# Kernel tuning notes

Measured on AMD Instinct MI355X. Metric: run time of the kernel, lower is better.

Reference implementation:

```python
import jax, jax.numpy as jnp
import numpy as np

B, N, K, D, H = 4, 8192, 16, 128, 4
DK = D // H  # key_dim = num_hiddens // num_heads
NEG_INF = -1e9


def setup_inputs() -> dict:
    key = jax.random.key(0)
    ks = jax.random.split(key, 16)
    s = 1.0 / np.sqrt(D)
    return {
        "vertex_feat": jax.random.normal(ks[0], (B, N, D), dtype=jnp.float32),
        "neighbors_idx": jax.random.randint(ks[1], (B, N, K), 0, N, dtype=jnp.int32),
        "valid_lens": jax.random.randint(ks[2], (B, N), 0, K, dtype=jnp.int32),
        # MultiHeadAttention projections (keras EinsumDense with bias)
        "Wq": (jax.random.normal(ks[3], (D, H, DK)) * s).astype(jnp.float32),
        "bq": jnp.zeros((H, DK), jnp.float32),
        "Wk": (jax.random.normal(ks[4], (D, H, DK)) * s).astype(jnp.float32),
        "bk": jnp.zeros((H, DK), jnp.float32),
        "Wv": (jax.random.normal(ks[5], (D, H, DK)) * s).astype(jnp.float32),
        "bv": jnp.zeros((H, DK), jnp.float32),
        "Wo": (jax.random.normal(ks[6], (H, DK, D)) * s).astype(jnp.float32),
        "bo": jnp.zeros((D,), jnp.float32),
        # MLP: Dense(D, relu) -> Dense(D)
        "W1": (jax.random.normal(ks[7], (D, D)) * s).astype(jnp.float32),
        "b1": jnp.zeros((D,), jnp.float32),
        "W2": (jax.random.normal(ks[8], (D, D)) * s).astype(jnp.float32),
        "b2": jnp.zeros((D,), jnp.float32),
    }


def reference(vertex_feat, neighbors_idx, valid_lens,
              Wq, bq, Wk, bk, Wv, bv, Wo, bo, W1, b1, W2, b2):
    # query: [B, N, 1, D]; gathered neighbors (batch_dims=1): [B, N, K, D]
    q = vertex_feat[:, :, None, :]
    neigh = jax.vmap(lambda vf, idx: vf[idx])(vertex_feat, neighbors_idx)
    value = jnp.concatenate([q, neigh], axis=2)  # [B, N, K+1, D]

    # per-head projections
    qh = jnp.einsum('bnqd,dhk->bnqhk', q, Wq) + bq      # [B,N,1,H,DK]
    kh = jnp.einsum('bnsd,dhk->bnshk', value, Wk) + bk  # [B,N,K+1,H,DK]
    vh = jnp.einsum('bnsd,dhk->bnshk', value, Wv) + bv

    # attention over the neighbor axis (attention_axes=(2,))
    scores = jnp.einsum('bnqhk,bnshk->bnhqs', qh, kh) / np.sqrt(DK)  # [B,N,H,1,K+1]
    # mask: positions < valid_lens + 1 (self + valid neighbors)
    pos = jnp.arange(K + 1)[None, None, :]                # [1,1,K+1]
    mask = pos < (valid_lens + 1)[:, :, None]             # [B,N,K+1] bool
    scores = scores + jnp.where(mask, 0.0, NEG_INF)[:, :, None, None, :]
    attn = jax.nn.softmax(scores, axis=-1)                # [B,N,H,1,K+1]

    ctx = jnp.einsum('bnhqs,bnshk->bnqhk', attn, vh)      # [B,N,1,H,DK]
    out = jnp.einsum('bnqhk,hkd->bnqd', ctx, Wo) + bo     # [B,N,1,D]
    out = out[:, :, 0, :]                                  # squeeze -> [B,N,D]

    # MLP (dropout inactive at inference)
    h = jax.nn.relu(out @ W1 + b1)
    new_vertex_feat = h @ W2 + b2
    return new_vertex_feat
```

## Files before the change

### kernel.cpp

```cpp
#include <hip/hip_runtime.h>
#include <math.h>

#define BB 4
#define NN 8192
#define KNB 16
#define DD 128
#define SS 17
#define M_TOT (BB*NN)
#define WPAD 136

typedef __attribute__((ext_vector_type(8))) short          bf8;
typedef __attribute__((ext_vector_type(4))) float          f4;
typedef __attribute__((ext_vector_type(4))) unsigned short u16x4;

static __device__ __forceinline__ unsigned short f2bf(float f) {
    unsigned u = __builtin_bit_cast(unsigned, f);
    u += 0x7fffu + ((u >> 16) & 1u);
    return (unsigned short)(u >> 16);
}
static __device__ __forceinline__ float bf2f_s(short h) {
    return __builtin_bit_cast(float, (unsigned)(unsigned short)h << 16);
}

__global__ __launch_bounds__(256) void cvt_wT(
    const float* __restrict__ Wq, const float* __restrict__ Wk,
    const float* __restrict__ Wv, const float* __restrict__ Wo,
    const float* __restrict__ W1, const float* __restrict__ W2,
    unsigned short* __restrict__ out)
{
    int m = blockIdx.x >> 4;
    const float* src = (m == 0) ? Wq : (m == 1) ? Wk : (m == 2) ? Wv
                     : (m == 3) ? Wo : (m == 4) ? W1 : W2;
    unsigned short* dst = out + m * 16384;
    int o = (blockIdx.x & 15) * 1024 + threadIdx.x * 4;
    int n = o >> 7, k = o & 127;
    u16x4 r;
    #pragma unroll
    for (int i = 0; i < 4; ++i) r[i] = f2bf(src[(size_t)(k + i) * 128 + n]);
    *(u16x4*)(dst + o) = r;
}

__global__ __launch_bounds__(256) void qkv_kernel(
    const float* __restrict__ X, const unsigned short* __restrict__ WtT,
    const float* __restrict__ bq, const float* __restrict__ bk,
    const float* __restrict__ bv,
    unsigned short* __restrict__ qh, unsigned short* __restrict__ kv)
{
    __shared__ unsigned short Xs[64 * WPAD];
    __shared__ unsigned short Wb[128 * WPAD];

    const int tid  = threadIdx.x;
    const int row0 = blockIdx.x * 64;

    {
        const float4* Xg = (const float4*)(X + (size_t)row0 * DD);
        #pragma unroll
        for (int i = 0; i < 8; ++i) {
            int idx = tid + i * 256;
            int r = idx >> 5, c4 = idx & 31;
            float4 v = Xg[idx];
            u16x4 u;
            u[0] = f2bf(v.x); u[1] = f2bf(v.y); u[2] = f2bf(v.z); u[3] = f2bf(v.w);
            *(u16x4*)(Xs + r * WPAD + c4 * 4) = u;
        }
    }
    #pragma unroll
    for (int i = 0; i < 8; ++i) {
        int c = tid + i * 256;
        int n = c >> 4, k8 = c & 15;
        *(bf8*)(Wb + n * WPAD + k8 * 8) = ((const bf8*)WtT)[c];
    }

    const int lane = tid & 63, wv = tid >> 6;
    const int ln = lane & 15, quad = lane >> 4;
    __syncthreads();

    bf8 afr[4];
    #pragma unroll
    for (int s = 0; s < 4; ++s)
        afr[s] = *(const bf8*)(Xs + (wv * 16 + ln) * WPAD + s * 32 + quad * 8);

    const float* biases[3] = { bq, bk, bv };
    unsigned short* outs[3] = { qh, kv, kv + 128 };
    const int strides[3] = { 128, 256, 256 };

    #pragma unroll 1
    for (int g = 0; g < 3; ++g) {
        if (g > 0) {
            __syncthreads();
            const bf8* Wn = (const bf8*)(WtT + g * 16384);
            #pragma unroll
            for (int i = 0; i < 8; ++i) {
                int c = tid + i * 256;
                int n = c >> 4, k8 = c & 15;
                *(bf8*)(Wb + n * WPAD + k8 * 8) = Wn[c];
            }
            __syncthreads();
        }

        f4 acc[8] = {};
        #pragma unroll
        for (int t = 0; t < 8; ++t) {
            bf8 bfr[4];
            #pragma unroll
            for (int s = 0; s < 4; ++s)
                bfr[s] = *(const bf8*)(Wb + (t * 16 + ln) * WPAD + s * 32 + quad * 8);
            #pragma unroll
            for (int s = 0; s < 4; ++s)
                acc[t] = __builtin_amdgcn_mfma_f32_16x16x32_bf16(afr[s], bfr[s], acc[t], 0, 0, 0);
        }

        const float* bias = biases[g];
        unsigned short* Y = outs[g];
        const int st = strides[g];
        #pragma unroll
        for (int t = 0; t < 8; ++t) {
            int col = t * 16 + ln;
            float bc = bias[col];
            #pragma unroll
            for (int r = 0; r < 4; ++r) {
                int row = row0 + wv * 16 + quad * 4 + r;
                Y[(size_t)row * st + col] = f2bf(acc[t][r] + bc);
            }
        }
    }
}

__global__ __launch_bounds__(256) void attn_kernel(
    const unsigned short* __restrict__ Qh, const unsigned short* __restrict__ KV,
    const int* __restrict__ nbr, const int* __restrict__ vlen,
    unsigned short* __restrict__ Ctx)
{
    const int tid  = threadIdx.x;
    const int vloc = tid >> 5;
    const int sp   = (tid >> 4) & 1;
    const int ln16 = tid & 15;
    const int blk  = blockIdx.x;
    const int b    = (blk & 7) >> 1;
    const int j    = ((blk >> 3) << 1) | (blk & 1);
    const int v    = b * NN + j * 8 + vloc;
    const int len  = vlen[v];

    bf8 q8 = *(const bf8*)(Qh + (size_t)v * DD + ln16 * 8);
    float qf[8];
    #pragma unroll
    for (int i = 0; i < 8; ++i) qf[i] = bf2f_s(q8[i]);

    int rows[9];
    {
        const int4* np = (const int4*)(nbr + (size_t)v * KNB);
        if (sp == 0) {
            rows[0] = v;
            int4 a = np[0], c = np[1];
            rows[1] = b * NN + a.x; rows[2] = b * NN + a.y;
            rows[3] = b * NN + a.z; rows[4] = b * NN + a.w;
            rows[5] = b * NN + c.x; rows[6] = b * NN + c.y;
            rows[7] = b * NN + c.z; rows[8] = b * NN + c.w;
        } else {
            int4 a = np[2], c = np[3];
            rows[0] = b * NN + a.x; rows[1] = b * NN + a.y;
            rows[2] = b * NN + a.z; rows[3] = b * NN + a.w;
            rows[4] = b * NN + c.x; rows[5] = b * NN + c.y;
            rows[6] = b * NN + c.z; rows[7] = b * NN + c.w;
            rows[8] = v;
        }
    }
    const int s0 = sp * 9;

    bf8 k8[9];
    #pragma unroll
    for (int i = 0; i < 9; ++i)
        k8[i] = *(const bf8*)(KV + (size_t)rows[i] * 256 + ln16 * 8);

    float sc[9];
    #pragma unroll
    for (int i = 0; i < 9; ++i) {
        float p = 0.f;
        #pragma unroll
        for (int d = 0; d < 8; ++d) p = fmaf(qf[d], bf2f_s(k8[i][d]), p);
        p += __shfl_xor(p, 1, 4);
        p += __shfl_xor(p, 2, 4);
        sc[i] = (s0 + i <= len) ? p * 0.17677669529663687f : -1.0e9f;
    }

    bf8 v8[9];
    #pragma unroll
    for (int i = 0; i < 9; ++i)
        v8[i] = *(const bf8*)(KV + (size_t)rows[i] * 256 + 128 + ln16 * 8);

    float m = sc[0];
    #pragma unroll
    for (int i = 1; i < 9; ++i) m = fmaxf(m, sc[i]);
    m = fmaxf(m, __shfl_xor(m, 16));
    float sum = 0.f;
    #pragma unroll
    for (int i = 0; i < 9; ++i) {
        float e = __expf(sc[i] - m);
        sc[i] = e;
        sum += e;
    }
    sum += __shfl_xor(sum, 16);
    const float inv = 1.f / sum;

    float acc[8] = {};
    #pragma unroll
    for (int i = 0; i < 9; ++i) {
        float w = sc[i] * inv;
        #pragma unroll
        for (int d = 0; d < 8; ++d) acc[d] = fmaf(w, bf2f_s(v8[i][d]), acc[d]);
    }
    #pragma unroll
    for (int d = 0; d < 8; ++d) acc[d] += __shfl_xor(acc[d], 16);

    if (sp == 0) {
        bf8 r;
        #pragma unroll
        for (int d = 0; d < 8; ++d) r[d] = (short)f2bf(acc[d]);
        *(bf8*)(Ctx + (size_t)v * DD + ln16 * 8) = r;
    }
}

__global__ __launch_bounds__(256) void ffn_kernel(
    const unsigned short* __restrict__ Ctxg, const unsigned short* __restrict__ WtT3,
    const float* __restrict__ bo, const float* __restrict__ b1,
    const float* __restrict__ b2, float* __restrict__ Out)
{
    __shared__ unsigned short Ct[64 * WPAD];
    __shared__ unsigned short Wb[128 * WPAD];

    const int tid  = threadIdx.x;
    const int row0 = blockIdx.x * 64;

    {
        const bf8* Cg = (const bf8*)(Ctxg + (size_t)row0 * DD);
        #pragma unroll
        for (int i = 0; i < 4; ++i) {
            int idx = tid + i * 256;
            int r = idx >> 4, c8 = idx & 15;
            *(bf8*)(Ct + r * WPAD + c8 * 8) = Cg[idx];
        }
    }
    #pragma unroll
    for (int i = 0; i < 8; ++i) {
        int c = tid + i * 256;
        int n = c >> 4, k8 = c & 15;
        *(bf8*)(Wb + n * WPAD + k8 * 8) = ((const bf8*)WtT3)[c];
    }

    const int lane = tid & 63, wv = tid >> 6;
    const int ln = lane & 15, quad = lane >> 4;
    const float* biases[3] = { bo, b1, b2 };
    __syncthreads();

    #pragma unroll 1
    for (int g = 0; g < 3; ++g) {
        bf8 afr[4];
        #pragma unroll
        for (int s = 0; s < 4; ++s)
            afr[s] = *(const bf8*)(Ct + (wv * 16 + ln) * WPAD + s * 32 + quad * 8);

        f4 acc[8] = {};
        #pragma unroll
        for (int t = 0; t < 8; ++t) {
            bf8 bfr[4];
            #pragma unroll
            for (int s = 0; s < 4; ++s)
                bfr[s] = *(const bf8*)(Wb + (t * 16 + ln) * WPAD + s * 32 + quad * 8);
            #pragma unroll
            for (int s = 0; s < 4; ++s)
                acc[t] = __builtin_amdgcn_mfma_f32_16x16x32_bf16(afr[s], bfr[s], acc[t], 0, 0, 0);
        }

        __syncthreads();

        const float* bias = biases[g];
        if (g == 2) {
            #pragma unroll
            for (int t = 0; t < 8; ++t) {
                int col = t * 16 + ln;
                float bc = bias[col];
                #pragma unroll
                for (int r = 0; r < 4; ++r) {
                    int row = row0 + wv * 16 + quad * 4 + r;
                    Out[(size_t)row * DD + col] = acc[t][r] + bc;
                }
            }
        } else {
            const bf8* Wn = (const bf8*)(WtT3 + (g + 1) * 16384);
            #pragma unroll
            for (int i = 0; i < 8; ++i) {
                int c = tid + i * 256;
                int n = c >> 4, k8 = c & 15;
                *(bf8*)(Wb + n * WPAD + k8 * 8) = Wn[c];
            }
            #pragma unroll
            for (int t = 0; t < 8; ++t) {
                int col = t * 16 + ln;
                float bc = bias[col];
                #pragma unroll
                for (int r = 0; r < 4; ++r) {
                    int rloc = wv * 16 + quad * 4 + r;
                    float vv = acc[t][r] + bc;
                    if (g == 1) vv = fmaxf(vv, 0.f);
                    Ct[rloc * WPAD + col] = f2bf(vv);
                }
            }
            __syncthreads();
        }
    }
}

extern "C" void kernel_launch(void* const* d_in, const int* in_sizes, int n_in,
                              void* d_out, int out_size, void* d_ws, size_t ws_size,
                              hipStream_t stream)
{
    const float* vf   = (const float*)d_in[0];
    const int*   nbr  = (const int*)  d_in[1];
    const int*   vlen = (const int*)  d_in[2];
    const float* Wq   = (const float*)d_in[3];
    const float* bq   = (const float*)d_in[4];
    const float* Wk   = (const float*)d_in[5];
    const float* bk   = (const float*)d_in[6];
    const float* Wv   = (const float*)d_in[7];
    const float* bv   = (const float*)d_in[8];
    const float* Wo   = (const float*)d_in[9];
    const float* bo   = (const float*)d_in[10];
    const float* W1   = (const float*)d_in[11];
    const float* b1   = (const float*)d_in[12];
    const float* W2   = (const float*)d_in[13];
    const float* b2   = (const float*)d_in[14];

    float* out = (float*)d_out;

    const size_t SZ = (size_t)M_TOT * DD;
    unsigned short* WtT = (unsigned short*)d_ws;
    unsigned short* qh  = WtT + 6 * 16384;
    unsigned short* kv  = qh + SZ;
    unsigned short* ctx = kv + 2 * SZ;

    cvt_wT<<<96, 256, 0, stream>>>(Wq, Wk, Wv, Wo, W1, W2, WtT);

    qkv_kernel<<<M_TOT / 64, 256, 0, stream>>>(vf, WtT, bq, bk, bv, qh, kv);

    attn_kernel<<<M_TOT / 8, 256, 0, stream>>>(qh, kv, nbr, vlen, ctx);

    ffn_kernel<<<M_TOT / 64, 256, 0, stream>>>(ctx, WtT + 3 * 16384, bo, b1, b2, out);
}
```

Baseline: 136.0 us.

## Fold output projection into first MLP layer via precomputed Wo·W1 product

Precomputes the product of the attention output projection and the first MLP weight (and the folded bias bo·W1+b1) using extra blocks in the QKV kernel. The FFN kernel then runs two GEMMs instead of three, removing one GEMM pass and one shared-memory round trip per row tile. It adds a tiny weight-product workload and changes rounding, since the combined matrix is stored in bf16.

```diff
diff --git a/kernel.cpp b/kernel.cpp
--- a/kernel.cpp
+++ b/kernel.cpp
@@ -28,29 +28,100 @@
     const float* __restrict__ W1, const float* __restrict__ W2,
     unsigned short* __restrict__ out)
 {
-    int m = blockIdx.x >> 4;
-    const float* src = (m == 0) ? Wq : (m == 1) ? Wk : (m == 2) ? Wv
-                     : (m == 3) ? Wo : (m == 4) ? W1 : W2;
-    unsigned short* dst = out + m * 16384;
-    int o = (blockIdx.x & 15) * 1024 + threadIdx.x * 4;
-    int n = o >> 7, k = o & 127;
-    u16x4 r;
-    #pragma unroll
-    for (int i = 0; i < 4; ++i) r[i] = f2bf(src[(size_t)(k + i) * 128 + n]);
-    *(u16x4*)(dst + o) = r;
+    const int blk = blockIdx.x;
+    if (blk < 96) {
+        int m = blk >> 4;
+        const float* src = (m == 0) ? Wq : (m == 1) ? Wk : (m == 2) ? Wv
+                         : (m == 3) ? Wo : (m == 4) ? W1 : W2;
+        unsigned short* dst = out + m * 16384;
+        int o = (blk & 15) * 1024 + threadIdx.x * 4;
+        int n = o >> 7, k = o & 127;
+        u16x4 r;
+        #pragma unroll
+        for (int i = 0; i < 4; ++i) r[i] = f2bf(src[(size_t)(k + i) * 128 + n]);
+        *(u16x4*)(dst + o) = r;
+    } else {
+        int o = (blk - 96) * 1024 + threadIdx.x * 4;
+        float4 v = *(const float4*)(Wo + o);
+        u16x4 r;
+        r[0] = f2bf(v.x); r[1] = f2bf(v.y); r[2] = f2bf(v.z); r[3] = f2bf(v.w);
+        *(u16x4*)(out + 6 * 16384 + o) = r;
+    }
 }
 
 __global__ __launch_bounds__(256) void qkv_kernel(
     const float* __restrict__ X, const unsigned short* __restrict__ WtT,
     const float* __restrict__ bq, const float* __restrict__ bk,
     const float* __restrict__ bv,
-    unsigned short* __restrict__ qh, unsigned short* __restrict__ kv)
+    const float* __restrict__ W1f, const float* __restrict__ bo,
+    const float* __restrict__ b1,
+    unsigned short* __restrict__ qh, unsigned short* __restrict__ kv,
+    unsigned short* __restrict__ WmT, float* __restrict__ bm)
 {
     __shared__ unsigned short Xs[64 * WPAD];
     __shared__ unsigned short Wb[128 * WPAD];
 
-    const int tid  = threadIdx.x;
-    const int row0 = blockIdx.x * 64;
+    const int tid = threadIdx.x;
+    const int blk = blockIdx.x;
+
+    if (blk >= 512) {
+        if (blk == 514) {
+            if (tid < 128) {
+                float a = b1[tid];
+                for (int d = 0; d < 128; ++d)
+                    a = fmaf(bo[d], W1f[(size_t)d * 128 + tid], a);
+                bm[tid] = a;
+            }
+            return;
+        }
+        const int row0 = (blk - 512) * 64;
+        {
+            const bf8* Ag = (const bf8*)(WtT + 4 * 16384 + (size_t)row0 * 128);
+            #pragma unroll
+            for (int i = 0; i < 4; ++i) {
+                int idx = tid + i * 256;
+                int r = idx >> 4, c8 = idx & 15;
+                *(bf8*)(Xs + r * WPAD + c8 * 8) = Ag[idx];
+            }
+            const bf8* Bg = (const bf8*)(WtT + 6 * 16384);
+            #pragma unroll
+            for (int i = 0; i < 8; ++i) {
+                int c = tid + i * 256;
+                int n = c >> 4, k8 = c & 15;
+                *(bf8*)(Wb + n * WPAD + k8 * 8) = Bg[c];
+            }
+        }
+        __syncthreads();
+        const int lane = tid & 63, wv = tid >> 6;
+        const int ln = lane & 15, quad = lane >> 4;
+        bf8 afr[4];
+        #pragma unroll
+        for (int s = 0; s < 4; ++s)
+            afr[s] = *(const bf8*)(Xs + (wv * 16 + ln) * WPAD + s * 32 + quad * 8);
+        f4 acc[8] = {};
+        #pragma unroll
+        for (int t = 0; t < 8; ++t) {
+            bf8 bfr[4];
+            #pragma unroll
+            for (int s = 0; s < 4; ++s)
+                bfr[s] = *(const bf8*)(Wb + (t * 16 + ln) * WPAD + s * 32 + quad * 8);
+            #pragma unroll
+            for (int s = 0; s < 4; ++s)
+                acc[t] = __builtin_amdgcn_mfma_f32_16x16x32_bf16(afr[s], bfr[s], acc[t], 0, 0, 0);
+        }
+        #pragma unroll
+        for (int t = 0; t < 8; ++t) {
+            int col = t * 16 + ln;
+            #pragma unroll
+            for (int r = 0; r < 4; ++r) {
+                int row = row0 + wv * 16 + quad * 4 + r;
+                WmT[(size_t)row * 128 + col] = f2bf(acc[t][r]);
+            }
+        }
+        return;
+    }
+
+    const int row0 = blk * 64;
 
     {
         const float4* Xg = (const float4*)(X + (size_t)row0 * DD);
@@ -221,8 +292,8 @@
 }
 
 __global__ __launch_bounds__(256) void ffn_kernel(
-    const unsigned short* __restrict__ Ctxg, const unsigned short* __restrict__ WtT3,
-    const float* __restrict__ bo, const float* __restrict__ b1,
+    const unsigned short* __restrict__ Ctxg, const unsigned short* __restrict__ WmT,
+    const unsigned short* __restrict__ W2T, const float* __restrict__ bm,
     const float* __restrict__ b2, float* __restrict__ Out)
 {
     __shared__ unsigned short Ct[64 * WPAD];
@@ -244,16 +315,14 @@
     for (int i = 0; i < 8; ++i) {
         int c = tid + i * 256;
         int n = c >> 4, k8 = c & 15;
-        *(bf8*)(Wb + n * WPAD + k8 * 8) = ((const bf8*)WtT3)[c];
+        *(bf8*)(Wb + n * WPAD + k8 * 8) = ((const bf8*)WmT)[c];
     }
 
     const int lane = tid & 63, wv = tid >> 6;
     const int ln = lane & 15, quad = lane >> 4;
-    const float* biases[3] = { bo, b1, b2 };
     __syncthreads();
 
-    #pragma unroll 1
-    for (int g = 0; g < 3; ++g) {
+    {
         bf8 afr[4];
         #pragma unroll
         for (int s = 0; s < 4; ++s)
@@ -273,39 +342,53 @@
 
         __syncthreads();
 
-        const float* bias = biases[g];
-        if (g == 2) {
-            #pragma unroll
-            for (int t = 0; t < 8; ++t) {
-                int col = t * 16 + ln;
-                float bc = bias[col];
-                #pragma unroll
-                for (int r = 0; r < 4; ++r) {
-                    int row = row0 + wv * 16 + quad * 4 + r;
-                    Out[(size_t)row * DD + col] = acc[t][r] + bc;
-                }
-            }
-        } else {
-            const bf8* Wn = (const bf8*)(WtT3 + (g + 1) * 16384);
-            #pragma unroll
-            for (int i = 0; i < 8; ++i) {
-                int c = tid + i * 256;
-                int n = c >> 4, k8 = c & 15;
-                *(bf8*)(Wb + n * WPAD + k8 * 8) = Wn[c];
-            }
-            #pragma unroll
-            for (int t = 0; t < 8; ++t) {
-                int col = t * 16 + ln;
-                float bc = bias[col];
-                #pragma unroll
-                for (int r = 0; r < 4; ++r) {
-                    int rloc = wv * 16 + quad * 4 + r;
-                    float vv = acc[t][r] + bc;
-                    if (g == 1) vv = fmaxf(vv, 0.f);
-                    Ct[rloc * WPAD + col] = f2bf(vv);
-                }
-            }
-            __syncthreads();
+        #pragma unroll
+        for (int i = 0; i < 8; ++i) {
+            int c = tid + i * 256;
+            int n = c >> 4, k8 = c & 15;
+            *(bf8*)(Wb + n * WPAD + k8 * 8) = ((const bf8*)W2T)[c];
+        }
+        #pragma unroll
+        for (int t = 0; t < 8; ++t) {
+            int col = t * 16 + ln;
+            float bc = bm[col];
+            #pragma unroll
+            for (int r = 0; r < 4; ++r) {
+                int rloc = wv * 16 + quad * 4 + r;
+                float vv = fmaxf(acc[t][r] + bc, 0.f);
+                Ct[rloc * WPAD + col] = f2bf(vv);
+            }
+        }
+        __syncthreads();
+    }
+
+    {
+        bf8 afr[4];
+        #pragma unroll
+        for (int s = 0; s < 4; ++s)
+            afr[s] = *(const bf8*)(Ct + (wv * 16 + ln) * WPAD + s * 32 + quad * 8);
+
+        f4 acc[8] = {};
+        #pragma unroll
+        for (int t = 0; t < 8; ++t) {
+            bf8 bfr[4];
+            #pragma unroll
+            for (int s = 0; s < 4; ++s)
+                bfr[s] = *(const bf8*)(Wb + (t * 16 + ln) * WPAD + s * 32 + quad * 8);
+            #pragma unroll
+            for (int s = 0; s < 4; ++s)
+                acc[t] = __builtin_amdgcn_mfma_f32_16x16x32_bf16(afr[s], bfr[s], acc[t], 0, 0, 0);
+        }
+
+        #pragma unroll
+        for (int t = 0; t < 8; ++t) {
+            int col = t * 16 + ln;
+            float bc = b2[col];
+            #pragma unroll
+            for (int r = 0; r < 4; ++r) {
+                int row = row0 + wv * 16 + quad * 4 + r;
+                Out[(size_t)row * DD + col] = acc[t][r] + bc;
+            }
         }
     }
 }
@@ -334,15 +417,18 @@
 
     const size_t SZ = (size_t)M_TOT * DD;
     unsigned short* WtT = (unsigned short*)d_ws;
-    unsigned short* qh  = WtT + 6 * 16384;
+    unsigned short* WmT = WtT + 7 * 16384;
+    float*          bm  = (float*)(WmT + 16384);
+    unsigned short* qh  = (unsigned short*)(bm + 128);
     unsigned short* kv  = qh + SZ;
     unsigned short* ctx = kv + 2 * SZ;
 
-    cvt_wT<<<96, 256, 0, stream>>>(Wq, Wk, Wv, Wo, W1, W2, WtT);
-
-    qkv_kernel<<<M_TOT / 64, 256, 0, stream>>>(vf, WtT, bq, bk, bv, qh, kv);
+    cvt_wT<<<112, 256, 0, stream>>>(Wq, Wk, Wv, Wo, W1, W2, WtT);
+
+    qkv_kernel<<<515, 256, 0, stream>>>(vf, WtT, bq, bk, bv, W1, bo, b1,
+                                        qh, kv, WmT, bm);
 
     attn_kernel<<<M_TOT / 8, 256, 0, stream>>>(qh, kv, nbr, vlen, ctx);
 
-    ffn_kernel<<<M_TOT / 64, 256, 0, stream>>>(ctx, WtT + 3 * 16384, bo, b1, b2, out);
-}
+    ffn_kernel<<<M_TOT / 64, 256, 0, stream>>>(ctx, WmT, WtT + 5 * 16384, bm, b2, out);
+}
```

Measured after the change: 135.6 us. About the same (-0.3%).
